# Performance work log

Measured on AMD Instinct MI355X. Metric: run time of the kernel, lower is better.

The kernel has to match this reference:

```python
import jax, jax.numpy as jnp
import numpy as np

B, N, C = 4, 32768, 64
D_IN = B * C          # 256 == in_channels * batch_size
D_MODEL = 256
HEADS = 2
NUM_EDGES = 4096
N_INC = 131072
EPS = 1e-5
NEG = 0.2


def _leaky(v):
    return jnp.where(v >= 0, v, NEG * v)


def _bn(v, g, b, m, var):  # BatchNorm1d, eval mode (running stats)
    return g * (v - m) * jax.lax.rsqrt(var + EPS) + b


def setup_inputs() -> dict:
    key = jax.random.key(0)
    ks = jax.random.split(key, 16)

    def lin_init(k, fan_in, shape):
        lim = 1.0 / np.sqrt(fan_in)
        return jax.random.uniform(k, shape, jnp.float32, -lim, lim)

    x = jax.random.normal(ks[0], (B, N, C), jnp.float32)
    row_n = jax.random.randint(ks[1], (N_INC,), 0, N, jnp.int32)
    row_e = jax.random.randint(ks[2], (N_INC,), 0, NUM_EDGES, jnp.int32)
    row_e = row_e.at[0].set(NUM_EDGES - 1)  # guarantee max edge id -> num_edges
    hyperedge_all = jnp.stack([row_n, row_e])

    return {
        "x": x,
        "hyperedge_all": hyperedge_all,
        # linear1: d_in -> d_model
        "W1": lin_init(ks[3], D_IN, (D_MODEL, D_IN)),
        "b1": lin_init(ks[4], D_IN, (D_MODEL,)),
        "bn1_g": 1.0 + 0.1 * jax.random.normal(ks[5], (D_MODEL,), jnp.float32),
        "bn1_b": 0.1 * jax.random.normal(ks[6], (D_MODEL,), jnp.float32),
        "bn1_m": 0.01 * jax.random.normal(ks[7], (D_MODEL,), jnp.float32),
        "bn1_v": jnp.ones((D_MODEL,), jnp.float32),
        # HypergraphConv lin: d_model -> heads*d_model (no bias); att: [heads, 2*d_model]
        "attW": lin_init(ks[8], D_MODEL, (HEADS * D_MODEL, D_MODEL)),
        "att": 0.1 * jax.random.normal(ks[9], (HEADS, 2 * D_MODEL), jnp.float32),
        "cb": 0.01 * jax.random.normal(ks[10], (D_MODEL,), jnp.float32),
        "bn2_g": 1.0 + 0.1 * jax.random.normal(ks[11], (D_MODEL,), jnp.float32),
        "bn2_b": 0.1 * jax.random.normal(ks[12], (D_MODEL,), jnp.float32),
        "bn2_m": 0.01 * jax.random.normal(ks[13], (D_MODEL,), jnp.float32),
        "bn2_v": jnp.ones((D_MODEL,), jnp.float32),
        # linear2: d_model -> d_in
        "W2": lin_init(ks[14], D_MODEL, (D_IN, D_MODEL)),
        "b2": lin_init(ks[15], D_MODEL, (D_IN,)),
        "ln_g": jnp.ones((C,), jnp.float32),
        "ln_b": jnp.zeros((C,), jnp.float32),
    }


def reference(x, hyperedge_all, W1, b1, bn1_g, bn1_b, bn1_m, bn1_v,
              attW, att, cb, bn2_g, bn2_b, bn2_m, bn2_v, W2, b2, ln_g, ln_b):
    src = x
    h = x.reshape(N, B * C)                               # [N, D_IN] (raw row-major reshape, as torch)
    h = _leaky(h @ W1.T + b1)                             # [N, D_MODEL]
    h = _bn(h, bn1_g, bn1_b, bn1_m, bn1_v)

    idx_n = hyperedge_all[0]                              # [I] node index per incidence
    idx_e = hyperedge_all[1]                              # [I] hyperedge index per incidence

    # hyperedge_attr = A^T h where A is the (0/1, duplicate-summed) incidence matrix
    eattr = jax.ops.segment_sum(h[idx_n], idx_e, NUM_EDGES)            # [E, D_MODEL]

    # --- HypergraphConv with attention, concat=False ---
    xh = (h @ attW.T).reshape(N, HEADS, D_MODEL)                       # [N, H, D]
    ea = (eattr @ attW.T).reshape(NUM_EDGES, HEADS, D_MODEL)           # [E, H, D]
    att_n, att_e = att[:, :D_MODEL], att[:, D_MODEL:]                  # [H, D] each
    sn = jnp.einsum('nhd,hd->nh', xh, att_n)                           # node score
    se = jnp.einsum('ehd,hd->eh', ea, att_e)                           # edge score
    alpha = _leaky(sn[idx_n] + se[idx_e])                              # [I, H]
    # segment softmax over destination nodes (PyG softmax(alpha, hyperedge_index[0]))
    amax = jax.ops.segment_max(alpha, idx_n, N)
    amax = jnp.where(jnp.isfinite(amax), amax, 0.0)
    ex = jnp.exp(alpha - amax[idx_n])
    denom = jax.ops.segment_sum(ex, idx_n, N)
    alpha = ex / (denom[idx_n] + 1e-16)                                # [I, H]

    ones_i = jnp.ones((N_INC,), h.dtype)
    deg_n = jax.ops.segment_sum(ones_i, idx_n, N)                      # D (hyperedge_weight = 1)
    Dinv = jnp.where(deg_n > 0, 1.0 / deg_n, 0.0)
    deg_e = jax.ops.segment_sum(ones_i, idx_e, NUM_EDGES)              # B
    Binv = jnp.where(deg_e > 0, 1.0 / deg_e, 0.0)

    # node -> edge: edge_out[e] = sum_inc B[e] * alpha * xh[n]
    m1 = Binv[idx_e][:, None, None] * alpha[:, :, None] * xh[idx_n]    # [I, H, D]
    edge_out = jax.ops.segment_sum(m1, idx_e, NUM_EDGES)               # [E, H, D]
    # edge -> node: node_out[n] = sum_inc D[n] * alpha * edge_out[e]
    m2 = Dinv[idx_n][:, None, None] * alpha[:, :, None] * edge_out[idx_e]
    node_out = jax.ops.segment_sum(m2, idx_n, N)                       # [N, H, D]
    x2 = node_out.mean(axis=1) + cb                                    # concat=False -> head mean + bias

    h = _bn(h + x2, bn2_g, bn2_b, bn2_m, bn2_v)
    h = _leaky(h @ W2.T + b2)                                          # [N, D_IN]

    y = src + h.reshape(B, N, C)                                       # residual (raw reshape back)
    mu = y.mean(-1, keepdims=True)                                     # LayerNorm over C
    var = jnp.mean((y - mu) ** 2, -1, keepdims=True)
    return ln_g * (y - mu) * jax.lax.rsqrt(var + EPS) + ln_b
```

## Files before the change

kernel.cpp:

```cpp
#include <hip/hip_runtime.h>

#define NN 32768
#define EE 4096
#define NI 131072
#define NEGS 0.2f
#define EPSV 1e-5f

typedef __bf16 bf16;
typedef __bf16 bf16x8 __attribute__((ext_vector_type(8)));
typedef __bf16 bf16x4 __attribute__((ext_vector_type(4)));
typedef float f32x4 __attribute__((ext_vector_type(4)));

#define AS1 __attribute__((address_space(1)))
#define AS3 __attribute__((address_space(3)))

__device__ __forceinline__ void gld16(const void* g, void* l) {
    __builtin_amdgcn_global_load_lds((const AS1 unsigned*)g, (AS3 unsigned*)l, 16, 0, 0);
}

__device__ __forceinline__ void stage_hl(const bf16* WH, const bf16* WL, bf16* sW,
                                         int buf, int kk, int wave, int lane) {
#pragma unroll
    for (int i = 0; i < 4; ++i) {
        size_t goff = (size_t)(wave*64 + lane)*256 + (size_t)kk*32 + i*8;
        size_t lb = (size_t)buf*16384 + (size_t)(i*256 + wave*64)*8;
        gld16(WH + goff, sW + lb);
        gld16(WL + goff, sW + 8192 + lb);
    }
}

__device__ __forceinline__ void stage_w(const bf16* WB, bf16* sW,
                                        int buf, int kk, int wave, int lane) {
#pragma unroll
    for (int i = 0; i < 4; ++i) {
        gld16(WB + (size_t)(wave*64 + lane)*256 + (size_t)kk*32 + i*8,
              sW + (size_t)buf*8192 + (size_t)(i*256 + wave*64)*8);
    }
}

constexpr size_t OFF_FLAGS = 0;
constexpr size_t OFF_W1F   = 32;
constexpr size_t OFF_WAF   = OFF_W1F + 65536;
constexpr size_t OFF_W2F   = OFF_WAF + 131072;
constexpr size_t OFF_SN    = OFF_W2F + 65536;
constexpr size_t OFF_SE    = OFF_SN + (size_t)NN*2;
constexpr size_t OFF_ALPHA = OFF_SE + (size_t)EE*2;
constexpr size_t OFF_DENOM = OFF_ALPHA + (size_t)NI*2;
constexpr size_t OFF_DEGN  = OFF_DENOM + (size_t)NN*2;
constexpr size_t OFF_DEGE  = OFF_DEGN + (size_t)NN;
constexpr size_t OFF_EATTR = OFF_DEGE + (size_t)EE;
constexpr size_t OFF_EOUT  = OFF_EATTR + (size_t)EE*256;
constexpr size_t OFF_H     = OFF_EOUT + (size_t)EE*512;
constexpr size_t OFF_WBA2  = OFF_H + (size_t)NN*256;
constexpr size_t OFF_WN    = OFF_WBA2 + 65536;
constexpr size_t OFF_WE    = OFF_WN + 512;
constexpr size_t OFF_ECOFF = OFF_WE + 512;
constexpr size_t OFF_ECURS = OFF_ECOFF + 4100;
constexpr size_t OFF_ECLIST= OFF_ECURS + (size_t)EE;
constexpr size_t WS_TOTAL  = OFF_ECLIST + (size_t)NI;

__device__ __forceinline__ float leaky(float v) { return v < 0.f ? NEGS * v : v; }

__device__ __forceinline__ float rdv(const void* p, size_t i, int f) {
    return f ? (float)((const bf16*)p)[i] : ((const float*)p)[i];
}

__device__ __forceinline__ void rd_idx(const void* p, int i, int mode, int& n, int& e) {
    if (mode == 0)      { n = ((const int*)p)[i];            e = ((const int*)p)[NI + i]; }
    else if (mode == 2) { n = ((const int*)p)[2*i];          e = ((const int*)p)[2*i + 1]; }
    else if (mode == 1) { n = (int)((const long long*)p)[i]; e = (int)((const long long*)p)[NI + i]; }
    else if (mode == 3) { n = (int)((const float*)p)[i];     e = (int)((const float*)p)[NI + i]; }
    else                { n = 0; e = 0; }
    if ((unsigned)n >= NN) n = 0;
    if ((unsigned)e >= EE) e = 0;
}

__global__ void detect_kernel(const void* p0, const void* p2, const void* p3, const void* p4,
                              const void* p5, const void* p6, const void* p7, const void* p8,
                              const void* p9, const void* p10, const void* p11, const void* p12,
                              const void* p13, const void* p14, const void* p15, const void* p16,
                              const void* p17, const void* p18, int* F) {
    __shared__ int cnt;
    int b = blockIdx.x, t = threadIdx.x;
    const void* ps[19] = {p0, nullptr, p2, p3, p4, p5, p6, p7, p8, p9, p10,
                          p11, p12, p13, p14, p15, p16, p17, p18};
    const int scan[19] = {2048, 0, 2048, 256, 256, 256, 256, 0, 2048, 1024,
                          256, 256, 256, 256, 0, 256, 256, 0, 0};
    if (b == 1)  { if (t == 0) { F[1] = 1; F[26] = 0; F[27] = 0; F[28] = 0; F[29] = 0; } return; }
    if (b == 18) { if (t == 0) F[18] = 1; return; }
    if (b == 7 || b == 14 || b == 17) {
        if (t == 0) F[b] = (*(const unsigned*)ps[b] == 0x3F803F80u) ? 1 : 0;
        return;
    }
    if (t == 0) cnt = 0;
    __syncthreads();
    int n = scan[b];
    int local = 0;
    for (int i = t; i < n; i += 256) {
        unsigned short u = ((const unsigned short*)ps[b])[i];
        if (((u >> 7) & 0xFFu) >= 0xC0u) local = 1;
    }
    if (local) atomicAdd(&cnt, 1);
    __syncthreads();
    if (t == 0) F[b] = (cnt == 0) ? 1 : 0;
}

__global__ void k_setflags(int* F) {
    if (threadIdx.x == 0) {
        F[25] = (!F[26]) ? 0 : (!F[28]) ? 2 : (!F[27]) ? 1 : (!F[29]) ? 3 : 99;
        int a = 1;
        const int ids[18] = {0,2,3,4,5,6,7,8,9,10,11,12,13,14,15,16,17,18};
        for (int k = 0; k < 18; ++k) a &= F[ids[k]];
        F[20] = a;
    }
}

__global__ void k_idxcheck(const void* p, int* F) {
    int i = blockIdx.x * 256 + threadIdx.x;
    const int*       p32 = (const int*)p;
    const long long* p64 = (const long long*)p;
    const float*     pf  = (const float*)p;
    int n0 = p32[i], e0 = p32[NI + i];
    if ((unsigned)n0 >= NN || (unsigned)e0 >= EE) atomicOr(&F[26], 1);
    int n2 = p32[2*i], e2 = p32[2*i + 1];
    if ((unsigned)n2 >= NN || (unsigned)e2 >= EE) atomicOr(&F[28], 1);
    long long n1 = p64[i], e1 = p64[NI + i];
    if (n1 < 0 || n1 >= NN || e1 < 0 || e1 >= EE) atomicOr(&F[27], 1);
    float nf = pf[i], ef = pf[NI + i];
    if (!(nf >= 0.f && nf < (float)NN && nf == floorf(nf)) ||
        !(ef >= 0.f && ef < (float)EE && ef == floorf(ef))) atomicOr(&F[29], 1);
}

__global__ void marker_kernel(float* OUT, int code) {
    size_t i = (size_t)blockIdx.x * 256 + threadIdx.x;
    OUT[i] = (i == 1) ? (float)code : 0.f;
}

__global__ void convb_kernel(const void* src, bf16* dst, const int* F, int fidx) {
    size_t i = ((size_t)blockIdx.x * 256 + threadIdx.x) * 4;
    if (F[fidx]) {
        *(bf16x4*)(dst + i) = *(const bf16x4*)((const bf16*)src + i);
    } else {
        f32x4 v = *(const f32x4*)((const float*)src + i);
        bf16x4 o;
        o[0] = (bf16)v[0]; o[1] = (bf16)v[1]; o[2] = (bf16)v[2]; o[3] = (bf16)v[3];
        *(bf16x4*)(dst + i) = o;
    }
}

__global__ void k_w1conv(const void* W1, const int* F, bf16* WH, bf16* WL) {
    size_t i = (size_t)blockIdx.x * 256 + threadIdx.x;
    float w = rdv(W1, i, F[2]);
    bf16 h = (bf16)w;
    WH[i] = h;
    WL[i] = (bf16)(w - (float)h);
}

__global__ void k_prep2(const void* g2, const void* be2, const void* m2, const void* v2,
                        const void* cb, const int* F, float* ST) {
    int k = threadIdx.x;
    float s = rdv(g2, k, F[11]) * rsqrtf(rdv(v2, k, F[14]) + EPSV);
    float t = s * (rdv(cb, k, F[10]) - rdv(m2, k, F[13])) + rdv(be2, k, F[12]);
    ST[k] = s; ST[256 + k] = t;
}

__global__ void k_w2conv(const void* W2, const void* b2, const float* ST, const int* F,
                         bf16* WH, bf16* WL, float* B2P) {
    __shared__ float sacc[4];
    int c = blockIdx.x, k = threadIdx.x;
    float w  = rdv(W2, (size_t)c*256 + k, F[15]);
    float sw = ST[k] * w;
    bf16 h = (bf16)sw;
    WH[(size_t)c*256 + k] = h;
    WL[(size_t)c*256 + k] = (bf16)(sw - (float)h);
    float p = ST[256 + k] * w;
#pragma unroll
    for (int m = 32; m >= 1; m >>= 1) p += __shfl_xor(p, m, 64);
    int lane = k & 63, wv = k >> 6;
    if (lane == 0) sacc[wv] = p;
    __syncthreads();
    if (k == 0) B2P[c] = rdv(b2, c, F[16]) + sacc[0] + sacc[1] + sacc[2] + sacc[3];
}

__global__ void k_fold(const void* attW, const void* att, const int* F,
                       float* WN, float* WE) {
    int c = threadIdx.x;
    int h = blockIdx.y;
    int d0 = blockIdx.x * 16;
    int faw = F[8], fat = F[9];
    float swn = 0.f, swe = 0.f;
#pragma unroll 4
    for (int dd = 0; dd < 16; ++dd) {
        int d = d0 + dd;
        float w = rdv(attW, (size_t)(h*256 + d)*256 + c, faw);
        swn += w * rdv(att, h*512 + d, fat);
        swe += w * rdv(att, h*512 + 256 + d, fat);
    }
    atomicAdd(&WN[h*256 + c], swn);
    atomicAdd(&WE[h*256 + c], swe);
}

__global__ void k_deg(const void* __restrict__ idx, float* __restrict__ DEGN,
                      float* __restrict__ DEGE, const int* __restrict__ F) {
    int i = blockIdx.x * 256 + threadIdx.x;
    int n, e; rd_idx(idx, i, F[25], n, e);
    atomicAdd(&DEGN[n], 1.f);
    atomicAdd(&DEGE[e], 1.f);
}

__global__ void scan_a(const float* __restrict__ DEGN, const float* __restrict__ DEGE,
                       int* __restrict__ BS) {
    __shared__ int wsum[4];
    int b = blockIdx.x, t = threadIdx.x, lane = t & 63, wave = t >> 6;
    const float* DEG = (b < 32) ? DEGN + (size_t)b*1024 : DEGE + (size_t)(b-32)*1024;
    f32x4 v = *(const f32x4*)(DEG + (size_t)t*4);
    int s = (int)v[0] + (int)v[1] + (int)v[2] + (int)v[3];
#pragma unroll
    for (int m = 32; m >= 1; m >>= 1) s += __shfl_xor(s, m, 64);
    if (lane == 0) wsum[wave] = s;
    __syncthreads();
    if (t == 0) BS[b] = wsum[0] + wsum[1] + wsum[2] + wsum[3];
}

__global__ void scan_b2(int* BS) {
    if (threadIdx.x == 0) { int run = 0; for (int i = 0;  i < 32; ++i) { int s = BS[i]; BS[i] = run; run += s; } }
    if (threadIdx.x == 1) { int run = 0; for (int i = 32; i < 36; ++i) { int s = BS[i]; BS[i] = run; run += s; } }
}

__global__ void scan_c(float* __restrict__ DEGN, float* __restrict__ DEGE,
                       const int* __restrict__ BS,
                       int* __restrict__ NOFF, int* __restrict__ NCURS,
                       int* __restrict__ ECOFF, int* __restrict__ ECURS) {
    __shared__ int wsum[4];
    int b = blockIdx.x, t = threadIdx.x, lane = t & 63, wave = t >> 6;
    bool isN = (b < 32);
    int bb = isN ? b : b - 32;
    float* DEG = isN ? DEGN + (size_t)bb*1024 : DEGE + (size_t)bb*1024;
    int* OFF   = isN ? NOFF + bb*1024 : ECOFF + bb*1024;
    int* CURS  = isN ? NCURS + bb*1024 : ECURS + bb*1024;
    f32x4 v = *(const f32x4*)(DEG + (size_t)t*4);
    int c0 = (int)v[0], c1 = (int)v[1], c2 = (int)v[2], c3 = (int)v[3];
    int s = c0 + c1 + c2 + c3;
    int p = s;
#pragma unroll
    for (int off = 1; off < 64; off <<= 1) {
        int u = __shfl_up(p, off, 64);
        if (lane >= off) p += u;
    }
    if (lane == 63) wsum[wave] = p;
    __syncthreads();
    int wb = 0;
    for (int w = 0; w < wave; ++w) wb += wsum[w];
    int run = BS[b] + wb + p - s;
    int i0 = t*4;
    int cs[4] = {c0, c1, c2, c3};
#pragma unroll
    for (int j = 0; j < 4; ++j) {
        OFF[i0 + j] = run; CURS[i0 + j] = run; run += cs[j];
        DEG[i0 + j] = cs[j] > 0 ? 1.f / (float)cs[j] : 0.f;
    }
    if (t == 255 && (b == 31 || b == 35)) OFF[1024] = run;
}

__global__ __launch_bounds__(256) void k_h_mfma(const void* __restrict__ x,
                                                const bf16* __restrict__ WH,
                                                const bf16* __restrict__ WL,
                                                const void* b1, const void* g1, const void* be1,
                                                const void* m1, const void* v1,
                                                const float* __restrict__ WN,
                                                const float* __restrict__ WE,
                                                const int* __restrict__ F,
                                                float* __restrict__ H,
                                                float* __restrict__ SN,
                                                float* __restrict__ HE) {
    __shared__ float sB[256], sA[256], sM[256], sBE[256];
    __shared__ float sWN0[256], sWN1[256], sWE0[256], sWE1[256];
    __shared__ __align__(16) bf16 sW[32768];
    int tid = threadIdx.x;
    {
        sB[tid]  = rdv(b1, tid, F[3]);
        sA[tid]  = rdv(g1, tid, F[4]) * rsqrtf(rdv(v1, tid, F[7]) + EPSV);
        sM[tid]  = rdv(m1, tid, F[6]);
        sBE[tid] = rdv(be1, tid, F[5]);
        sWN0[tid] = WN[tid];
        sWN1[tid] = WN[256 + tid];
        sWE0[tid] = WE[tid];
        sWE1[tid] = WE[256 + tid];
    }
    int lane = tid & 63, wave = tid >> 6;
    int l15 = lane & 15, quad = lane >> 4;
    int row0 = (blockIdx.x * 4 + wave) * 16;
    int fx = F[0];
    const size_t abase = (size_t)(row0 + l15) * 256;
    f32x4 acc[16];
#pragma unroll
    for (int t = 0; t < 16; ++t) acc[t] = (f32x4){0.f, 0.f, 0.f, 0.f};
    stage_hl(WH, WL, sW, 0, 0, wave, lane);
    bf16x8 aNb; f32x4 aN0, aN1;
    if (fx) {
        aNb = *(const bf16x8*)((const bf16*)x + abase + quad*8);
    } else {
        aN0 = *(const f32x4*)((const float*)x + abase + quad*8);
        aN1 = *(const f32x4*)((const float*)x + abase + quad*8 + 4);
    }
    __syncthreads();
    int cur = 0;
    for (int kk = 0; kk < 8; ++kk) {
        if (kk < 7) stage_hl(WH, WL, sW, cur ^ 1, kk + 1, wave, lane);
        bf16x8 ah, al;
        if (fx) {
            ah = aNb;
            if (kk < 7) aNb = *(const bf16x8*)((const bf16*)x + abase + (kk+1)*32 + quad*8);
        } else {
            f32x4 a0 = aN0, a1 = aN1;
            if (kk < 7) {
                aN0 = *(const f32x4*)((const float*)x + abase + (kk+1)*32 + quad*8);
                aN1 = *(const f32x4*)((const float*)x + abase + (kk+1)*32 + quad*8 + 4);
            }
#pragma unroll
            for (int j = 0; j < 4; ++j) {
                bf16 h0 = (bf16)a0[j]; ah[j] = h0; al[j] = (bf16)(a0[j] - (float)h0);
                bf16 h1 = (bf16)a1[j]; ah[4+j] = h1; al[4+j] = (bf16)(a1[j] - (float)h1);
            }
        }
        const bf16* pH = sW + cur*16384 + quad*2048 + l15*8;
        const bf16* pL = pH + 8192;
#pragma unroll
        for (int t = 0; t < 16; ++t) {
            bf16x8 bh = *(const bf16x8*)(pH + t*128);
            bf16x8 bl = *(const bf16x8*)(pL + t*128);
            acc[t] = __builtin_amdgcn_mfma_f32_16x16x32_bf16(ah, bh, acc[t], 0, 0, 0);
            if (!fx) acc[t] = __builtin_amdgcn_mfma_f32_16x16x32_bf16(al, bh, acc[t], 0, 0, 0);
            acc[t] = __builtin_amdgcn_mfma_f32_16x16x32_bf16(ah, bl, acc[t], 0, 0, 0);
        }
        __syncthreads();
        cur ^= 1;
    }
    float p0[4] = {0.f,0.f,0.f,0.f}, p1[4] = {0.f,0.f,0.f,0.f};
    float q0[4] = {0.f,0.f,0.f,0.f}, q1[4] = {0.f,0.f,0.f,0.f};
#pragma unroll
    for (int t = 0; t < 16; ++t) {
        int cc = t*16 + l15;
        float A = sA[cc], Mv = sM[cc], BE = sBE[cc], Bv = sB[cc];
        float wn0 = sWN0[cc], wn1 = sWN1[cc], we0 = sWE0[cc], we1 = sWE1[cc];
#pragma unroll
        for (int r = 0; r < 4; ++r) {
            int rr = row0 + quad*4 + r;
            float v = leaky(acc[t][r] + Bv);
            float hv = A * (v - Mv) + BE;
            H[(size_t)rr*256 + cc] = hv;
            p0[r] += hv * wn0;
            p1[r] += hv * wn1;
            q0[r] += hv * we0;
            q1[r] += hv * we1;
        }
    }
#pragma unroll
    for (int r = 0; r < 4; ++r) {
#pragma unroll
        for (int m = 8; m >= 1; m >>= 1) {
            p0[r] += __shfl_xor(p0[r], m, 64);
            p1[r] += __shfl_xor(p1[r], m, 64);
            q0[r] += __shfl_xor(q0[r], m, 64);
            q1[r] += __shfl_xor(q1[r], m, 64);
        }
        if (l15 == 0) {
            int rr = row0 + quad*4 + r;
            SN[(size_t)rr*2]     = p0[r];
            SN[(size_t)rr*2 + 1] = p1[r];
            HE[(size_t)rr*2]     = q0[r];
            HE[(size_t)rr*2 + 1] = q1[r];
        }
    }
}

__global__ void k_sefill(const void* __restrict__ idx, const float* __restrict__ HE,
                         float* __restrict__ SE, int* __restrict__ ECURS,
                         int* __restrict__ CLIST, const int* __restrict__ F) {
    int i = blockIdx.x * 256 + threadIdx.x;
    int n, e; rd_idx(idx, i, F[25], n, e);
    atomicAdd(&SE[(size_t)e*2],     HE[(size_t)n*2]);
    atomicAdd(&SE[(size_t)e*2 + 1], HE[(size_t)n*2 + 1]);
    int pos = atomicAdd(&ECURS[e], 1);
    CLIST[pos] = i;
}

__global__ void k_alpha(const void* idx, const float* SN, const float* SE,
                        float* ALPHA, float* DENOM, int* NCURS, int* NLIST, const int* F) {
    int i = blockIdx.x * 256 + threadIdx.x;
    int n, e; rd_idx(idx, i, F[25], n, e);
    float e0 = expf(leaky(SN[(size_t)n*2]     + SE[(size_t)e*2]));
    float e1 = expf(leaky(SN[(size_t)n*2 + 1] + SE[(size_t)e*2 + 1]));
    ALPHA[(size_t)i*2] = e0; ALPHA[(size_t)i*2 + 1] = e1;
    atomicAdd(&DENOM[(size_t)n*2], e0);
    atomicAdd(&DENOM[(size_t)n*2 + 1], e1);
    int pos = atomicAdd(&NCURS[n], 1);
    NLIST[pos] = i;
}

__global__ __launch_bounds__(256) void m1g_csr_k(const int* __restrict__ COFF,
                                                 const int* __restrict__ CLIST,
                                                 const void* __restrict__ idx,
                                                 const float* __restrict__ ALPHA,
                                                 const float* __restrict__ DENOM,
                                                 const float* __restrict__ H,
                                                 bf16* __restrict__ G,
                                                 const int* __restrict__ F) {
    __shared__ int   s_n[64];
    __shared__ float s_c0[64];
    __shared__ float s_c1[64];
    int e = blockIdx.x, t = threadIdx.x;
    int beg = COFF[e], end = COFF[e + 1];
    float acc0 = 0.f, acc1 = 0.f;
    for (int base = beg; base < end; base += 64) {
        int cnt = min(64, end - base);
        if (t < cnt) {
            int i = CLIST[base + t];
            int n, ee; rd_idx(idx, i, F[25], n, ee);
            s_n[t]  = n;
            s_c0[t] = ALPHA[(size_t)i*2]     / (DENOM[(size_t)n*2]     + 1e-16f);
            s_c1[t] = ALPHA[(size_t)i*2 + 1] / (DENOM[(size_t)n*2 + 1] + 1e-16f);
        }
        __syncthreads();
        for (int k = 0; k < cnt; ++k) {
            float hv = H[(size_t)s_n[k]*256 + t];
            acc0 += s_c0[k] * hv;
            acc1 += s_c1[k] * hv;
        }
        __syncthreads();
    }
    G[(size_t)e*512 + t]       = (bf16)acc0;
    G[(size_t)e*512 + 256 + t] = (bf16)acc1;
}

__global__ __launch_bounds__(256) void gemm_eout_k(const bf16* __restrict__ G,
                                                   const bf16* __restrict__ WBA,
                                                   const float* __restrict__ BINV,
                                                   bf16* __restrict__ EOUT) {
    __shared__ __align__(16) bf16 sW[16384];
    int h = blockIdx.y;
    int tid = threadIdx.x, lane = tid & 63, wave = tid >> 6;
    int l15 = lane & 15, quad = lane >> 4;
    int row0 = blockIdx.x * 16;
    const bf16* Arow = G + (size_t)(row0 + l15) * 512 + h * 256;
    const bf16* WB = WBA + (size_t)h * 65536;
    f32x4 acc[4];
#pragma unroll
    for (int t = 0; t < 4; ++t) acc[t] = (f32x4){0.f, 0.f, 0.f, 0.f};
    stage_w(WB, sW, 0, 0, wave, lane);
    bf16x8 aN = *(const bf16x8*)(Arow + quad*8);
    __syncthreads();
    int cur = 0;
    for (int kk = 0; kk < 8; ++kk) {
        if (kk < 7) stage_w(WB, sW, cur ^ 1, kk + 1, wave, lane);
        bf16x8 a = aN;
        if (kk < 7) aN = *(const bf16x8*)(Arow + (kk+1)*32 + quad*8);
        const bf16* pB = sW + cur*8192 + quad*2048 + l15*8;
#pragma unroll
        for (int tc = 0; tc < 4; ++tc) {
            int t = wave*4 + tc;
            bf16x8 b = *(const bf16x8*)(pB + t*128);
            acc[tc] = __builtin_amdgcn_mfma_f32_16x16x32_bf16(a, b, acc[tc], 0, 0, 0);
        }
        __syncthreads();
        cur ^= 1;
    }
#pragma unroll
    for (int tc = 0; tc < 4; ++tc) {
        int cc = (wave*4 + tc)*16 + l15;
#pragma unroll
        for (int r = 0; r < 4; ++r) {
            int e = row0 + quad*4 + r;
            EOUT[(size_t)e*512 + h*256 + cc] = (bf16)(acc[tc][r] * BINV[e]);
        }
    }
}

__global__ __launch_bounds__(256) void k_m2g(const int* __restrict__ NOFF,
                                             const int* __restrict__ NLIST,
                                             const void* __restrict__ idx,
                                             const float* __restrict__ ALPHA,
                                             const float* __restrict__ DENOM,
                                             const float* __restrict__ DINV,
                                             const bf16* __restrict__ EOUT,
                                             float* __restrict__ H,
                                             const int* __restrict__ F) {
    __shared__ int   s_e[64];
    __shared__ float s_a0[64];
    __shared__ float s_a1[64];
    int n = blockIdx.x, t = threadIdx.x;
    int beg = NOFF[n], end = NOFF[n + 1];
    float dn0 = DENOM[(size_t)n*2]     + 1e-16f;
    float dn1 = DENOM[(size_t)n*2 + 1] + 1e-16f;
    float acc = 0.f;
    for (int base = beg; base < end; base += 64) {
        int cnt = min(64, end - base);
        if (t < cnt) {
            int i = NLIST[base + t];
            int nn, e; rd_idx(idx, i, F[25], nn, e);
            s_e[t]  = e;
            s_a0[t] = ALPHA[(size_t)i*2]     / dn0;
            s_a1[t] = ALPHA[(size_t)i*2 + 1] / dn1;
        }
        __syncthreads();
        for (int k = 0; k < cnt; ++k) {
            int e = s_e[k];
            acc += s_a0[k] * (float)EOUT[(size_t)e*512 + t]
                 + s_a1[k] * (float)EOUT[(size_t)e*512 + 256 + t];
        }
        __syncthreads();
    }
    H[(size_t)n*256 + t] += 0.5f * DINV[n] * acc;
}

__global__ __launch_bounds__(256) void k_out_mfma(const float* __restrict__ H,
                                                  const bf16* __restrict__ WH,
                                                  const bf16* __restrict__ WL,
                                                  const float* __restrict__ B2P,
                                                  const void* __restrict__ x,
                                                  const void* lng, const void* lnb,
                                                  const int* __restrict__ F,
                                                  void* __restrict__ OUT) {
    __shared__ float sB2[256];
    __shared__ float sG[64], sBnd[64];
    __shared__ __align__(16) bf16 sW[32768];
    int tid = threadIdx.x;
    {
        sB2[tid] = B2P[tid];
        if (tid < 64) { sG[tid] = rdv(lng, tid, F[17]); sBnd[tid] = rdv(lnb, tid, F[18]); }
    }
    int lane = tid & 63, wave = tid >> 6;
    int l15 = lane & 15, quad = lane >> 4;
    int row0 = (blockIdx.x * 4 + wave) * 16;
    int fx = F[0], fo = F[20];
    const float* Arow = H + (size_t)(row0 + l15) * 256;
    f32x4 acc[16];
#pragma unroll
    for (int t = 0; t < 16; ++t) acc[t] = (f32x4){0.f, 0.f, 0.f, 0.f};
    stage_hl(WH, WL, sW, 0, 0, wave, lane);
    f32x4 aN0 = *(const f32x4*)(Arow + quad*8);
    f32x4 aN1 = *(const f32x4*)(Arow + quad*8 + 4);
    __syncthreads();
    int cur = 0;
    for (int kk = 0; kk < 8; ++kk) {
        if (kk < 7) stage_hl(WH, WL, sW, cur ^ 1, kk + 1, wave, lane);
        f32x4 a0 = aN0, a1 = aN1;
        if (kk < 7) {
            aN0 = *(const f32x4*)(Arow + (kk+1)*32 + quad*8);
            aN1 = *(const f32x4*)(Arow + (kk+1)*32 + quad*8 + 4);
        }
        bf16x8 ah, al;
#pragma unroll
        for (int j = 0; j < 4; ++j) {
            bf16 h0 = (bf16)a0[j]; ah[j] = h0; al[j] = (bf16)(a0[j] - (float)h0);
            bf16 h1 = (bf16)a1[j]; ah[4+j] = h1; al[4+j] = (bf16)(a1[j] - (float)h1);
        }
        const bf16* pH = sW + cur*16384 + quad*2048 + l15*8;
        const bf16* pL = pH + 8192;
#pragma unroll
        for (int t = 0; t < 16; ++t) {
            bf16x8 bh = *(const bf16x8*)(pH + t*128);
            bf16x8 bl = *(const bf16x8*)(pL + t*128);
            acc[t] = __builtin_amdgcn_mfma_f32_16x16x32_bf16(ah, bh, acc[t], 0, 0, 0);
            acc[t] = __builtin_amdgcn_mfma_f32_16x16x32_bf16(al, bh, acc[t], 0, 0, 0);
            acc[t] = __builtin_amdgcn_mfma_f32_16x16x32_bf16(ah, bl, acc[t], 0, 0, 0);
        }
        __syncthreads();
        cur ^= 1;
    }
#pragma unroll
    for (int t = 0; t < 16; ++t) {
        int cc = t*16 + l15;
        float Bv = sB2[cc];
#pragma unroll
        for (int r = 0; r < 4; ++r) {
            int rr = row0 + quad*4 + r;
            acc[t][r] = rdv(x, (size_t)rr*256 + cc, fx) + leaky(acc[t][r] + Bv);
        }
    }
#pragma unroll
    for (int r = 0; r < 4; ++r) {
        int rr = row0 + quad*4 + r;
#pragma unroll
        for (int g = 0; g < 4; ++g) {
            float s = acc[4*g][r] + acc[4*g+1][r] + acc[4*g+2][r] + acc[4*g+3][r];
            s += __shfl_xor(s, 1, 64); s += __shfl_xor(s, 2, 64);
            s += __shfl_xor(s, 4, 64); s += __shfl_xor(s, 8, 64);
            float mu = s * (1.f / 64.f);
            float q = 0.f;
#pragma unroll
            for (int j = 0; j < 4; ++j) { float d = acc[4*g+j][r] - mu; q += d * d; }
            q += __shfl_xor(q, 1, 64); q += __shfl_xor(q, 2, 64);
            q += __shfl_xor(q, 4, 64); q += __shfl_xor(q, 8, 64);
            float rsq = rsqrtf(q * (1.f / 64.f) + EPSV);
#pragma unroll
            for (int j = 0; j < 4; ++j) {
                int cc = (4*g + j)*16 + l15;
                int gi = cc & 63;
                float o = sG[gi] * (acc[4*g+j][r] - mu) * rsq + sBnd[gi];
                size_t idx = (size_t)rr*256 + cc;
                if (fo) ((bf16*)OUT)[idx] = (bf16)o;
                else    ((float*)OUT)[idx] = o;
            }
        }
    }
}

extern "C" void kernel_launch(void* const* d_in, const int* in_sizes, int n_in,
                              void* d_out, int out_size, void* d_ws, size_t ws_size,
                              hipStream_t stream) {
    float* ws = (float*)d_ws;
    int* F = (int*)(ws + OFF_FLAGS);

    if (ws_size < WS_TOTAL * sizeof(float)) {
        marker_kernel<<<NN, 256, 0, stream>>>((float*)d_out, 300);
        return;
    }
    if (n_in < 19) {
        marker_kernel<<<NN, 256, 0, stream>>>((float*)d_out, 355);
        return;
    }
    const int exp_sizes[19] = {8388608, 262144, 65536, 256, 256, 256, 256, 256, 131072,
                               1024, 256, 256, 256, 256, 256, 65536, 256, 64, 64};
    for (int i = 0; i < 19; ++i) {
        if (in_sizes[i] != exp_sizes[i]) {
            marker_kernel<<<NN, 256, 0, stream>>>((float*)d_out, 330 + i);
            return;
        }
    }

    float* ST    = ws + OFF_W1F;
    float* B2P   = ws + OFF_W1F + 512;
    int*   BS    = (int*)(ws + OFF_W1F + 768);
    int*   NCURS = (int*)(ws + OFF_W1F + 1024);
    int*   NOFF  = (int*)(ws + OFF_W2F);
    bf16*  W1H = (bf16*)(ws + OFF_WAF);
    bf16*  W1L = (bf16*)(ws + OFF_WAF + 32768);
    bf16*  W2H = (bf16*)(ws + OFF_WAF + 65536);
    bf16*  W2L = (bf16*)(ws + OFF_WAF + 98304);
    int*   ECOFF  = (int*)(ws + OFF_ECOFF);
    int*   ECURS  = (int*)(ws + OFF_ECURS);
    int*   CLIST  = (int*)(ws + OFF_ECLIST);
    float* HE     = ws + OFF_EATTR;
    int*   NLIST  = (int*)(ws + OFF_EATTR + 65536);
    bf16*  Gb     = (bf16*)(ws + OFF_EOUT);
    bf16*  EOUTb  = (bf16*)(ws + OFF_EOUT + 1048576);

    hipMemsetAsync((char*)d_ws + OFF_SE * 4, 0, (OFF_EATTR - OFF_SE) * 4, stream);
    hipMemsetAsync((char*)d_ws + OFF_WN * 4, 0, 1024 * 4, stream);

    detect_kernel<<<19, 256, 0, stream>>>(d_in[0], d_in[2], d_in[3], d_in[4], d_in[5], d_in[6],
                                          d_in[7], d_in[8], d_in[9], d_in[10], d_in[11], d_in[12],
                                          d_in[13], d_in[14], d_in[15], d_in[16], d_in[17], d_in[18], F);
    k_idxcheck<<<NI/256, 256, 0, stream>>>(d_in[1], F);
    k_setflags<<<1, 64, 0, stream>>>(F);

    k_deg<<<NI/256, 256, 0, stream>>>(d_in[1], ws + OFF_DEGN, ws + OFF_DEGE, F);
    scan_a<<<36, 256, 0, stream>>>(ws + OFF_DEGN, ws + OFF_DEGE, BS);
    scan_b2<<<1, 64, 0, stream>>>(BS);
    scan_c<<<36, 256, 0, stream>>>(ws + OFF_DEGN, ws + OFF_DEGE, BS, NOFF, NCURS, ECOFF, ECURS);

    k_w1conv<<<256, 256, 0, stream>>>(d_in[2], F, W1H, W1L);
    convb_kernel<<<128, 256, 0, stream>>>(d_in[8], (bf16*)(ws + OFF_WBA2), F, 8);
    k_fold<<<dim3(16, 2), 256, 0, stream>>>(d_in[8], d_in[9], F, ws + OFF_WN, ws + OFF_WE);
    k_prep2<<<1, 256, 0, stream>>>(d_in[11], d_in[12], d_in[13], d_in[14], d_in[10], F, ST);
    k_w2conv<<<256, 256, 0, stream>>>(d_in[15], d_in[16], ST, F, W2H, W2L, B2P);

    k_h_mfma<<<NN/64, 256, 0, stream>>>(d_in[0], W1H, W1L, d_in[3], d_in[4], d_in[5],
                                        d_in[6], d_in[7], ws + OFF_WN, ws + OFF_WE, F,
                                        ws + OFF_H, ws + OFF_SN, HE);
    k_sefill<<<NI/256, 256, 0, stream>>>(d_in[1], HE, ws + OFF_SE, ECURS, CLIST, F);
    k_alpha<<<NI/256, 256, 0, stream>>>(d_in[1], ws + OFF_SN, ws + OFF_SE, ws + OFF_ALPHA,
                                        ws + OFF_DENOM, NCURS, NLIST, F);

    m1g_csr_k<<<EE, 256, 0, stream>>>(ECOFF, CLIST, d_in[1], ws + OFF_ALPHA, ws + OFF_DENOM,
                                      ws + OFF_H, Gb, F);

    gemm_eout_k<<<dim3(EE/16, 2), 256, 0, stream>>>(Gb, (const bf16*)(ws + OFF_WBA2),
                                                    ws + OFF_DEGE, EOUTb);

    k_m2g<<<NN, 256, 0, stream>>>(NOFF, NLIST, d_in[1], ws + OFF_ALPHA, ws + OFF_DENOM,
                                  ws + OFF_DEGN, EOUTb, ws + OFF_H, F);
    k_out_mfma<<<NN/64, 256, 0, stream>>>(ws + OFF_H, W2H, W2L, B2P, d_in[0],
                                          d_in[17], d_in[18], F, d_out);
}
```

Before: 455.9 us.

## Halve LDS weight staging in MFMA GEMM kernels to raise occupancy

Both MFMA GEMM kernels now stage the weight tile in half-width phases: 128 output columns per phase, with 16 phases instead of 8 k-steps. This halves the shared-memory buffer from 64KB to 32KB and adds a launch-bounds hint for 4 blocks per CU, so more blocks can be resident at once. The BatchNorm affine is also folded into one multiply-add with a precomputed offset. In exchange there are twice as many barriers and smaller prefetch batches per phase, which may expose more load latency.

Result: no change. 461.7 us (+1.3%).

```diff
diff --git a/kernel.cpp b/kernel.cpp
--- a/kernel.cpp
+++ b/kernel.cpp
@@ -18,14 +18,17 @@
     __builtin_amdgcn_global_load_lds((const AS1 unsigned*)g, (AS3 unsigned*)l, 16, 0, 0);
 }
 
-__device__ __forceinline__ void stage_hl(const bf16* WH, const bf16* WL, bf16* sW,
-                                         int buf, int kk, int wave, int lane) {
-#pragma unroll
-    for (int i = 0; i < 4; ++i) {
-        size_t goff = (size_t)(wave*64 + lane)*256 + (size_t)kk*32 + i*8;
-        size_t lb = (size_t)buf*16384 + (size_t)(i*256 + wave*64)*8;
+__device__ __forceinline__ void stage_half(const bf16* WH, const bf16* WL, bf16* sW,
+                                           int buf, int phase, int tid) {
+    int kk = phase >> 1, h = phase & 1;
+#pragma unroll
+    for (int j = 0; j < 2; ++j) {
+        int m = j*256 + tid;
+        int i = m >> 7, rr = m & 127;
+        size_t goff = (size_t)(h*128 + rr)*256 + (size_t)kk*32 + i*8;
+        size_t lb = (size_t)buf*8192 + (size_t)m*8;
         gld16(WH + goff, sW + lb);
-        gld16(WL + goff, sW + 8192 + lb);
+        gld16(WL + goff, sW + 4096 + lb);
     }
 }
 
@@ -262,7 +265,7 @@
     if (t == 255 && (b == 31 || b == 35)) OFF[1024] = run;
 }
 
-__global__ __launch_bounds__(256) void k_h_mfma(const void* __restrict__ x,
+__global__ __launch_bounds__(256, 4) void k_h_mfma(const void* __restrict__ x,
                                                 const bf16* __restrict__ WH,
                                                 const bf16* __restrict__ WL,
                                                 const void* b1, const void* g1, const void* be1,
@@ -273,15 +276,15 @@
                                                 float* __restrict__ H,
                                                 float* __restrict__ SN,
                                                 float* __restrict__ HE) {
-    __shared__ float sB[256], sA[256], sM[256], sBE[256];
+    __shared__ float sB[256], sA[256], sC[256];
     __shared__ float sWN0[256], sWN1[256], sWE0[256], sWE1[256];
-    __shared__ __align__(16) bf16 sW[32768];
+    __shared__ __align__(16) bf16 sW[16384];
     int tid = threadIdx.x;
     {
-        sB[tid]  = rdv(b1, tid, F[3]);
-        sA[tid]  = rdv(g1, tid, F[4]) * rsqrtf(rdv(v1, tid, F[7]) + EPSV);
-        sM[tid]  = rdv(m1, tid, F[6]);
-        sBE[tid] = rdv(be1, tid, F[5]);
+        float A = rdv(g1, tid, F[4]) * rsqrtf(rdv(v1, tid, F[7]) + EPSV);
+        sB[tid] = rdv(b1, tid, F[3]);
+        sA[tid] = A;
+        sC[tid] = rdv(be1, tid, F[5]) - A * rdv(m1, tid, F[6]);
         sWN0[tid] = WN[tid];
         sWN1[tid] = WN[256 + tid];
         sWE0[tid] = WE[tid];
@@ -295,8 +298,9 @@
     f32x4 acc[16];
 #pragma unroll
     for (int t = 0; t < 16; ++t) acc[t] = (f32x4){0.f, 0.f, 0.f, 0.f};
-    stage_hl(WH, WL, sW, 0, 0, wave, lane);
+    stage_half(WH, WL, sW, 0, 0, tid);
     bf16x8 aNb; f32x4 aN0, aN1;
+    bf16x8 ah = {}, al = {};
     if (fx) {
         aNb = *(const bf16x8*)((const bf16*)x + abase + quad*8);
     } else {
@@ -305,30 +309,33 @@
     }
     __syncthreads();
     int cur = 0;
-    for (int kk = 0; kk < 8; ++kk) {
-        if (kk < 7) stage_hl(WH, WL, sW, cur ^ 1, kk + 1, wave, lane);
-        bf16x8 ah, al;
-        if (fx) {
-            ah = aNb;
-            if (kk < 7) aNb = *(const bf16x8*)((const bf16*)x + abase + (kk+1)*32 + quad*8);
-        } else {
-            f32x4 a0 = aN0, a1 = aN1;
-            if (kk < 7) {
-                aN0 = *(const f32x4*)((const float*)x + abase + (kk+1)*32 + quad*8);
-                aN1 = *(const f32x4*)((const float*)x + abase + (kk+1)*32 + quad*8 + 4);
+    for (int phase = 0; phase < 16; ++phase) {
+        if (phase < 15) stage_half(WH, WL, sW, cur ^ 1, phase + 1, tid);
+        int kk = phase >> 1, h = phase & 1;
+        if (h == 0) {
+            if (fx) {
+                ah = aNb;
+                if (kk < 7) aNb = *(const bf16x8*)((const bf16*)x + abase + (kk+1)*32 + quad*8);
+            } else {
+                f32x4 a0 = aN0, a1 = aN1;
+                if (kk < 7) {
+                    aN0 = *(const f32x4*)((const float*)x + abase + (kk+1)*32 + quad*8);
+                    aN1 = *(const f32x4*)((const float*)x + abase + (kk+1)*32 + quad*8 + 4);
+                }
+#pragma unroll
+                for (int j = 0; j < 4; ++j) {
+                    bf16 h0 = (bf16)a0[j]; ah[j] = h0; al[j] = (bf16)(a0[j] - (float)h0);
+                    bf16 h1 = (bf16)a1[j]; ah[4+j] = h1; al[4+j] = (bf16)(a1[j] - (float)h1);
+                }
             }
-#pragma unroll
-            for (int j = 0; j < 4; ++j) {
-                bf16 h0 = (bf16)a0[j]; ah[j] = h0; al[j] = (bf16)(a0[j] - (float)h0);
-                bf16 h1 = (bf16)a1[j]; ah[4+j] = h1; al[4+j] = (bf16)(a1[j] - (float)h1);
-            }
-        }
-        const bf16* pH = sW + cur*16384 + quad*2048 + l15*8;
-        const bf16* pL = pH + 8192;
-#pragma unroll
-        for (int t = 0; t < 16; ++t) {
-            bf16x8 bh = *(const bf16x8*)(pH + t*128);
-            bf16x8 bl = *(const bf16x8*)(pL + t*128);
+        }
+        const bf16* pH = sW + cur*8192 + quad*1024 + l15*8;
+        const bf16* pL = pH + 4096;
+#pragma unroll
+        for (int tl = 0; tl < 8; ++tl) {
+            int t = h*8 + tl;
+            bf16x8 bh = *(const bf16x8*)(pH + tl*128);
+            bf16x8 bl = *(const bf16x8*)(pL + tl*128);
             acc[t] = __builtin_amdgcn_mfma_f32_16x16x32_bf16(ah, bh, acc[t], 0, 0, 0);
             if (!fx) acc[t] = __builtin_amdgcn_mfma_f32_16x16x32_bf16(al, bh, acc[t], 0, 0, 0);
             acc[t] = __builtin_amdgcn_mfma_f32_16x16x32_bf16(ah, bl, acc[t], 0, 0, 0);
@@ -341,13 +348,12 @@
 #pragma unroll
     for (int t = 0; t < 16; ++t) {
         int cc = t*16 + l15;
-        float A = sA[cc], Mv = sM[cc], BE = sBE[cc], Bv = sB[cc];
+        float A = sA[cc], Cv = sC[cc], Bv = sB[cc];
         float wn0 = sWN0[cc], wn1 = sWN1[cc], we0 = sWE0[cc], we1 = sWE1[cc];
 #pragma unroll
         for (int r = 0; r < 4; ++r) {
             int rr = row0 + quad*4 + r;
-            float v = leaky(acc[t][r] + Bv);
-            float hv = A * (v - Mv) + BE;
+            float hv = A * leaky(acc[t][r] + Bv) + Cv;
             H[(size_t)rr*256 + cc] = hv;
             p0[r] += hv * wn0;
             p1[r] += hv * wn1;
@@ -513,7 +519,7 @@
     H[(size_t)n*256 + t] += 0.5f * DINV[n] * acc;
 }
 
-__global__ __launch_bounds__(256) void k_out_mfma(const float* __restrict__ H,
+__global__ __launch_bounds__(256, 4) void k_out_mfma(const float* __restrict__ H,
                                                   const bf16* __restrict__ WH,
                                                   const bf16* __restrict__ WL,
                                                   const float* __restrict__ B2P,
@@ -523,7 +529,7 @@
                                                   void* __restrict__ OUT) {
     __shared__ float sB2[256];
     __shared__ float sG[64], sBnd[64];
-    __shared__ __align__(16) bf16 sW[32768];
+    __shared__ __align__(16) bf16 sW[16384];
     int tid = threadIdx.x;
     {
         sB2[tid] = B2P[tid];
@@ -537,30 +543,34 @@
     f32x4 acc[16];
 #pragma unroll
     for (int t = 0; t < 16; ++t) acc[t] = (f32x4){0.f, 0.f, 0.f, 0.f};
-    stage_hl(WH, WL, sW, 0, 0, wave, lane);
+    stage_half(WH, WL, sW, 0, 0, tid);
     f32x4 aN0 = *(const f32x4*)(Arow + quad*8);
     f32x4 aN1 = *(const f32x4*)(Arow + quad*8 + 4);
+    bf16x8 ah = {}, al = {};
     __syncthreads();
     int cur = 0;
-    for (int kk = 0; kk < 8; ++kk) {
-        if (kk < 7) stage_hl(WH, WL, sW, cur ^ 1, kk + 1, wave, lane);
-        f32x4 a0 = aN0, a1 = aN1;
-        if (kk < 7) {
-            aN0 = *(const f32x4*)(Arow + (kk+1)*32 + quad*8);
-            aN1 = *(const f32x4*)(Arow + (kk+1)*32 + quad*8 + 4);
-        }
-        bf16x8 ah, al;
-#pragma unroll
-        for (int j = 0; j < 4; ++j) {
-            bf16 h0 = (bf16)a0[j]; ah[j] = h0; al[j] = (bf16)(a0[j] - (float)h0);
-            bf16 h1 = (bf16)a1[j]; ah[4+j] = h1; al[4+j] = (bf16)(a1[j] - (float)h1);
-        }
-        const bf16* pH = sW + cur*16384 + quad*2048 + l15*8;
-        const bf16* pL = pH + 8192;
-#pragma unroll
-        for (int t = 0; t < 16; ++t) {
-            bf16x8 bh = *(const bf16x8*)(pH + t*128);
-            bf16x8 bl = *(const bf16x8*)(pL + t*128);
+    for (int phase = 0; phase < 16; ++phase) {
+        if (phase < 15) stage_half(WH, WL, sW, cur ^ 1, phase + 1, tid);
+        int kk = phase >> 1, h = phase & 1;
+        if (h == 0) {
+            f32x4 a0 = aN0, a1 = aN1;
+            if (kk < 7) {
+                aN0 = *(const f32x4*)(Arow + (kk+1)*32 + quad*8);
+                aN1 = *(const f32x4*)(Arow + (kk+1)*32 + quad*8 + 4);
+            }
+#pragma unroll
+            for (int j = 0; j < 4; ++j) {
+                bf16 h0 = (bf16)a0[j]; ah[j] = h0; al[j] = (bf16)(a0[j] - (float)h0);
+                bf16 h1 = (bf16)a1[j]; ah[4+j] = h1; al[4+j] = (bf16)(a1[j] - (float)h1);
+            }
+        }
+        const bf16* pH = sW + cur*8192 + quad*1024 + l15*8;
+        const bf16* pL = pH + 4096;
+#pragma unroll
+        for (int tl = 0; tl < 8; ++tl) {
+            int t = h*8 + tl;
+            bf16x8 bh = *(const bf16x8*)(pH + tl*128);
+            bf16x8 bl = *(const bf16x8*)(pL + tl*128);
             acc[t] = __builtin_amdgcn_mfma_f32_16x16x32_bf16(ah, bh, acc[t], 0, 0, 0);
             acc[t] = __builtin_amdgcn_mfma_f32_16x16x32_bf16(al, bh, acc[t], 0, 0, 0);
             acc[t] = __builtin_amdgcn_mfma_f32_16x16x32_bf16(ah, bl, acc[t], 0, 0, 0);
```
